# Kernel tuning notes

Hardware: AMD Instinct MI355X
Metric: run time of the kernel (lower is better)

## Reference

```python
import jax, jax.numpy as jnp
import numpy as np

B, C, H, W = 16, 512, 64, 64

def setup_inputs() -> dict:
    key = jax.random.key(0)
    k1, k2, k3 = jax.random.split(key, 3)
    x = jax.random.normal(k1, (B, C, H, W), dtype=jnp.float32)
    gamma = jnp.zeros((1,), dtype=jnp.float32)
    W1 = jax.random.normal(k2, (C, C // 8), dtype=jnp.float32) * (1.0 / np.sqrt(C))
    b1 = jnp.zeros((C // 8,), dtype=jnp.float32)
    W2 = jax.random.normal(k3, (C // 8, C), dtype=jnp.float32) * (1.0 / np.sqrt(C // 8))
    b2 = jnp.zeros((C,), dtype=jnp.float32)
    return {"x": x, "gamma": gamma, "W1": W1, "b1": b1, "W2": W2, "b2": b2}

def reference(x, gamma, W1, b1, W2, b2):
    b, c, h, w = x.shape
    q = x.reshape(b, c, h * w)                      # B,C,HW
    energy = jnp.einsum('bcn,bdn->bcd', q, q)       # B,C,C
    energy_new = jnp.max(energy, axis=-1, keepdims=True) - energy
    attention = jax.nn.softmax(energy_new, axis=-1)
    ch_out = jnp.einsum('bcd,bdn->bcn', attention, q).reshape(b, c, h, w)
    # SE branch: global avg pool -> Linear -> ReLU -> Linear -> Sigmoid
    se = jnp.mean(x, axis=(2, 3))                   # B,C
    se = jax.nn.relu(se @ W1 + b1)
    se = jax.nn.sigmoid(se @ W2 + b2)               # B,C
    out = gamma * (ch_out * se[:, :, None, None]) + x
    return out
```

## Files before the change

kernel.cpp:

```cpp
#include <hip/hip_runtime.h>
#include <cstdint>
#include <cstddef>

#define B_ 16
#define C_ 512
#define N_ 4096
#define CH_ 64

#define VMWAIT(n) asm volatile("s_waitcnt vmcnt(" #n ")" ::: "memory")
#define LGKM0()   asm volatile("s_waitcnt lgkmcnt(0)" ::: "memory")
#define BARRAW()  asm volatile("s_barrier" ::: "memory")
#define SCHEDBAR() __builtin_amdgcn_sched_barrier(0)

typedef __attribute__((ext_vector_type(8))) short short8;
typedef __attribute__((ext_vector_type(4))) short short4t;
typedef __attribute__((ext_vector_type(4))) float f32x4;

__device__ __forceinline__ unsigned short f2bf(float f) {
  union { float f; unsigned u; } v; v.f = f;
  unsigned r = v.u + 0x7FFFu + ((v.u >> 16) & 1u);
  return (unsigned short)(r >> 16);
}
__device__ __forceinline__ float bf2f(unsigned short u) {
  union { unsigned u; float f; } v; v.u = ((unsigned)u) << 16;
  return v.f;
}
__device__ __forceinline__ ushort4 cvt4(float4 v) {
  ushort4 u; u.x = f2bf(v.x); u.y = f2bf(v.y); u.z = f2bf(v.z); u.w = f2bf(v.w);
  return u;
}
__device__ __forceinline__ void gload_lds16(const void* g, void* l) {
  __builtin_amdgcn_global_load_lds((__attribute__((address_space(1))) void*)g,
                                   (__attribute__((address_space(3))) void*)l,
                                   16, 0, 0);
}
__device__ __forceinline__ unsigned lds_off(const void* p) {
  return (unsigned)(size_t)(__attribute__((address_space(3))) const char*)p;
}

template <int CPW>
__device__ __forceinline__ void stage_pair(
    const unsigned short* __restrict__ Asrc, const unsigned short* __restrict__ Bsrc,
    char* Adst, char* Bdst, int t, int ko, bool doB) {
  const int l = t & 63, wid = t >> 6;
  const int srow = l >> 3, scc = l & 7;
#pragma unroll
  for (int i = 0; i < CPW; ++i) {
    const int chunk = wid * CPW + i;
    const int row = chunk * 8 + srow;
    const int cc = scc ^ (row & 7);
    gload_lds16(Asrc + (size_t)row * N_ + ko + cc * 8, Adst + chunk * 1024);
    if (doB)
      gload_lds16(Bsrc + (size_t)row * N_ + ko + cc * 8, Bdst + chunk * 1024);
  }
}
template <int MF, int NF>
__device__ __forceinline__ void gemm_step_t(const char* Abase, const char* Bbase,
                                            int l, int wA, int wB,
                                            f32x4 (&acc)[MF][NF]) {
#pragma unroll
  for (int ks = 0; ks < 2; ++ks) {
    short8 af[MF], bfv[NF];
#pragma unroll
    for (int m = 0; m < MF; ++m) {
      const int row = wA * (MF * 16) + m * 16 + (l & 15);
      const int ch = (ks * 4 + (l >> 4)) ^ (row & 7);
      af[m] = *(const short8*)(Abase + row * 128 + ch * 16);
    }
#pragma unroll
    for (int n = 0; n < NF; ++n) {
      const int row = wB * (NF * 16) + n * 16 + (l & 15);
      const int ch = (ks * 4 + (l >> 4)) ^ (row & 7);
      bfv[n] = *(const short8*)(Bbase + row * 128 + ch * 16);
    }
#pragma unroll
    for (int m = 0; m < MF; ++m)
#pragma unroll
      for (int n = 0; n < NF; ++n)
        acc[m][n] = __builtin_amdgcn_mfma_f32_16x16x32_bf16(af[m], bfv[n],
                                                            acc[m][n], 0, 0, 0);
  }
}

__device__ __forceinline__ void stage_att_half(
    const unsigned short* __restrict__ src, char* dst, int t, int ko, int h) {
  const int l = t & 63, wid = t >> 6;
  const int srow = l >> 3, scc = l & 7;
#pragma unroll
  for (int i = 0; i < 2; ++i) {
    const int chunk = h * 16 + wid * 2 + i;
    const int row = chunk * 8 + srow;
    const int cc = scc ^ (row & 7);
    gload_lds16(src + (size_t)row * C_ + ko + cc * 8, dst + chunk * 1024);
  }
}
__device__ __forceinline__ void stage_q_half(
    const unsigned short* __restrict__ src,
    char* dst, int t, int h) {
  const int l = t & 63, wid = t >> 6;
  const int dd = (l >> 1) & 3;
  const int nb = (l >> 3) * 16 + (l & 1) * 8;
#pragma unroll
  for (int i = 0; i < 2; ++i) {
    const int chunk = h * 16 + wid * 2 + i;
    gload_lds16(src + (size_t)((chunk >> 1) * 4 + dd) * N_ + (chunk & 1) * 128 + nb,
                dst + chunk * 1024);
  }
}

template <int KS>
__device__ __forceinline__ void load_af(const char* Qc, int l, int wn2,
                                        short4t (&lo)[8], short4t (&hi)[8]) {
  const unsigned base = lds_off(Qc) + KS * 16384 + (unsigned)((l >> 4) * 4096 +
                        wn2 * 1024 + (l & 15) * 2);
#pragma unroll
  for (int nf = 0; nf < 8; ++nf) {
    const unsigned a = base + nf * 128;
    asm volatile("ds_read_b64_tr_b16 %0, %2\n\t"
                 "ds_read_b64_tr_b16 %1, %2 offset:2048"
                 : "=&v"(lo[nf]), "=&v"(hi[nf]) : "v"(a));
  }
}
template <int KS, int CB>
__device__ __forceinline__ void load_bf(const char* Pc, int l, int wc,
                                        short8 (&bf)[2]) {
#pragma unroll
  for (int cf = 0; cf < 2; ++cf) {
    const int c_l = CB * 128 + wc * 32 + cf * 16 + (l & 15);
    bf[cf] = *(const short8*)(Pc + c_l * 128 +
                              (((KS * 4 + (l >> 4)) ^ (c_l & 7)) * 16));
  }
}
template <int CB>
__device__ __forceinline__ void mfma16(const short8 (&af)[8], const short8 (&bf)[2],
                                       f32x4 (&acc)[8][4]) {
  __builtin_amdgcn_s_setprio(1);
#pragma unroll
  for (int nf = 0; nf < 8; ++nf)
#pragma unroll
    for (int cf = 0; cf < 2; ++cf)
      acc[nf][CB * 2 + cf] = __builtin_amdgcn_mfma_f32_16x16x32_bf16(
          af[nf], bf[cf], acc[nf][CB * 2 + cf], 0, 0, 0);
  __builtin_amdgcn_s_setprio(0);
}

__global__ __launch_bounds__(256) void k1_convert(
    const float* __restrict__ x, unsigned short* __restrict__ qbf,
    float* __restrict__ partial) {
  __shared__ float wsum[4];
  const size_t base = (size_t)blockIdx.x * N_;
  const int t = threadIdx.x;
  float s = 0.f;
#pragma unroll
  for (int k = 0; k < 4; ++k) {
    const int idx = (t + k * 256) * 4;
    float4 v = *(const float4*)(x + base + idx);
    *(ushort4*)(qbf + base + idx) = cvt4(v);
    s += (v.x + v.y) + (v.z + v.w);
  }
#pragma unroll
  for (int o = 1; o < 64; o <<= 1) s += __shfl_xor(s, o);
  if ((t & 63) == 0) wsum[t >> 6] = s;
  __syncthreads();
  if (t == 0) partial[blockIdx.x] = (wsum[0] + wsum[1]) + (wsum[2] + wsum[3]);
}

__global__ __launch_bounds__(256) void k2_se(
    const float* __restrict__ partial, const float* __restrict__ gamma,
    const float* __restrict__ W1, const float* __restrict__ b1,
    const float* __restrict__ W2, const float* __restrict__ b2,
    float* __restrict__ gse) {
  __shared__ float se_s[C_];
  __shared__ float hp[4][CH_];
  __shared__ float h_s[CH_];
  const int b = blockIdx.x, t = threadIdx.x;
  for (int c = t; c < C_; c += 256)
    se_s[c] = partial[b * C_ + c] * (1.0f / (float)N_);
  __syncthreads();
  {
    const int h = t & 63, seg = t >> 6;
    float a = 0.f;
    const int cb = seg * 128;
    for (int c = cb; c < cb + 128; ++c) a += se_s[c] * W1[c * CH_ + h];
    hp[seg][h] = a;
  }
  __syncthreads();
  if (t < CH_) {
    float a = b1[t] + hp[0][t] + hp[1][t] + hp[2][t] + hp[3][t];
    h_s[t] = fmaxf(a, 0.f);
  }
  __syncthreads();
  const float g = gamma[0];
  for (int c = t; c < C_; c += 256) {
    float a = b2[c];
#pragma unroll
    for (int hh = 0; hh < CH_; ++hh) a += h_s[hh] * W2[hh * C_ + c];
    const float sig = 1.0f / (1.0f + __expf(-a));
    gse[b * C_ + c] = g * sig;
  }
}

__global__ __launch_bounds__(512) void k3_energy(
    const unsigned short* __restrict__ qbf, float* __restrict__ ep) {
  __shared__ alignas(16) char lds[65536];
  const int orig = blockIdx.x;
  const int wg = (orig & 7) * 80 + (orig >> 3);
  const int b = wg / 40;
  const int rem = wg % 40;
  const int kc = rem / 10;
  const int tid = rem % 10;
  int i, j;
  if (tid < 4)      { i = 0; j = tid; }
  else if (tid < 7) { i = 1; j = tid - 3; }
  else if (tid < 9) { i = 2; j = tid - 5; }
  else              { i = 3; j = 3; }
  const int c0 = i * 128, d0 = j * 128;
  const bool diag = (i == j);
  const unsigned short* qb = qbf + (size_t)b * C_ * N_ + kc * 1024;
  const int t = threadIdx.x, l = t & 63, wid = t >> 6;
  const int wd = wid >> 1, wcc = wid & 1;
  f32x4 acc[2][4];
#pragma unroll
  for (int m = 0; m < 2; ++m)
#pragma unroll
    for (int n = 0; n < 4; ++n) acc[m][n] = (f32x4){0.f, 0.f, 0.f, 0.f};
  char* A0 = lds;             char* B0 = lds + 16384;
  char* A1 = lds + 32768;     char* B1 = lds + 49152;
  const unsigned short* cp = qb + (size_t)c0 * N_;
  const unsigned short* dp = qb + (size_t)d0 * N_;

  stage_pair<2>(cp, dp, A0, B0, t, 0, !diag);
  for (int kt = 0; kt < 16; ++kt) {
    char* curA = (kt & 1) ? A1 : A0;
    char* curB = (kt & 1) ? B1 : B0;
    char* nxtA = (kt & 1) ? A0 : A1;
    char* nxtB = (kt & 1) ? B0 : B1;
    if (kt < 15) {
      stage_pair<2>(cp, dp, nxtA, nxtB, t, (kt + 1) * 64, !diag);
      if (diag) { VMWAIT(2); } else { VMWAIT(4); }
    } else {
      VMWAIT(0);
    }
    BARRAW();
    gemm_step_t<2, 4>(diag ? curA : curB, curA, l, wd, wcc, acc);
    BARRAW();
  }

  float* Lf = (float*)lds;
  float* eb = ep + ((size_t)(kc * B_ + b)) * C_ * C_;
#pragma unroll
  for (int df = 0; df < 2; ++df)
#pragma unroll
    for (int cf = 0; cf < 4; ++cf) {
      const int c_l = wcc * 64 + cf * 16 + (l & 15);
      const int d4 = wd * 32 + df * 16 + ((l >> 4) << 2);
      *(float4*)&Lf[c_l * 128 + (d4 ^ ((c_l & 7) << 2))] =
          *(const float4*)&acc[df][cf];
    }
  __syncthreads();
#pragma unroll
  for (int jj = 0; jj < 8; ++jj) {
    const int row = jj * 16 + (t >> 5);
    const int col4 = (t & 31) * 4;
    float4 v = *(const float4*)&Lf[row * 128 + (col4 ^ ((row & 7) << 2))];
    *(float4*)&eb[(size_t)(c0 + row) * C_ + d0 + col4] = v;
  }
  if (!diag) {
    __syncthreads();
#pragma unroll
    for (int df = 0; df < 2; ++df)
#pragma unroll
      for (int cf = 0; cf < 4; ++cf) {
        const int c_l = wcc * 64 + cf * 16 + (l & 15);
#pragma unroll
        for (int r = 0; r < 4; ++r) {
          const int d_l = wd * 32 + df * 16 + ((l >> 4) << 2) + r;
          Lf[d_l * 128 + (c_l ^ ((d_l & 7) << 2))] = acc[df][cf][r];
        }
      }
    __syncthreads();
#pragma unroll
    for (int jj = 0; jj < 8; ++jj) {
      const int row = jj * 16 + (t >> 5);
      const int col4 = (t & 31) * 4;
      float4 v = *(const float4*)&Lf[row * 128 + (col4 ^ ((row & 7) << 2))];
      *(float4*)&eb[(size_t)(d0 + row) * C_ + c0 + col4] = v;
    }
  }
}

__global__ __launch_bounds__(256) void k4_softmax(const float* __restrict__ ep,
                                                  unsigned short* __restrict__ att) {
  const int t = threadIdx.x, l = t & 63, wid = t >> 6;
  const size_t row = (size_t)blockIdx.x * 4 + wid;
  f32x4 v0 = (f32x4){0.f, 0.f, 0.f, 0.f}, v1 = v0;
#pragma unroll
  for (int k = 0; k < 4; ++k) {
    const f32x4* er = (const f32x4*)(ep + ((size_t)k * B_ * C_ + row) * C_);
    v0 += er[l];
    v1 += er[64 + l];
  }
  float mn = fminf(fminf(fminf(v0[0], v0[1]), fminf(v0[2], v0[3])),
                   fminf(fminf(v1[0], v1[1]), fminf(v1[2], v1[3])));
#pragma unroll
  for (int s = 1; s < 64; s <<= 1) mn = fminf(mn, __shfl_xor(mn, s));
  float e0 = __expf(mn - v0[0]), e1 = __expf(mn - v0[1]);
  float e2 = __expf(mn - v0[2]), e3 = __expf(mn - v0[3]);
  float e4 = __expf(mn - v1[0]), e5 = __expf(mn - v1[1]);
  float e6 = __expf(mn - v1[2]), e7 = __expf(mn - v1[3]);
  float sm = ((e0 + e1) + (e2 + e3)) + ((e4 + e5) + (e6 + e7));
#pragma unroll
  for (int s = 1; s < 64; s <<= 1) sm += __shfl_xor(sm, s);
  const float inv = 1.0f / sm;
  unsigned short* ar = att + row * C_;
  ushort4 u0, u1;
  u0.x = f2bf(e0 * inv); u0.y = f2bf(e1 * inv);
  u0.z = f2bf(e2 * inv); u0.w = f2bf(e3 * inv);
  u1.x = f2bf(e4 * inv); u1.y = f2bf(e5 * inv);
  u1.z = f2bf(e6 * inv); u1.w = f2bf(e7 * inv);
  *(ushort4*)(ar + 4 * l) = u0;
  *(ushort4*)(ar + 256 + 4 * l) = u1;
}

__global__ __launch_bounds__(512) void k5_pv(
    const unsigned short* __restrict__ att, const unsigned short* __restrict__ qbf,
    const float* __restrict__ gse, float* __restrict__ out) {
  __shared__ alignas(16) char lds[131072];
  const int orig = blockIdx.x;
  const int wg = (orig & 7) * 64 + (orig >> 3);
  const int b = wg >> 5;
  const int rem = wg & 31;
  const int c0 = (rem & 1) * 256, n0 = (rem >> 1) * 256;
  const int t = threadIdx.x, l = t & 63, wid = t >> 6;
  const int wn2 = wid >> 2, wc = wid & 3;
  const unsigned short* ab = att + (size_t)b * C_ * C_ + (size_t)c0 * C_;
  const unsigned short* qb = qbf + (size_t)b * C_ * N_ + n0;
  f32x4 acc[8][4];
#pragma unroll
  for (int m = 0; m < 8; ++m)
#pragma unroll
    for (int n = 0; n < 4; ++n) acc[m][n] = (f32x4){0.f, 0.f, 0.f, 0.f};
  char* P0 = lds;            char* P1 = lds + 32768;
  char* Q0 = lds + 65536;    char* Q1 = lds + 98304;

  short4t lo[8], hi[8];
  short8 af[8], bf[2];

  stage_att_half(ab, P0, t, 0, 0);
  stage_att_half(ab, P0, t, 0, 1);
  stage_q_half(qb, Q0, t, 0);
  stage_q_half(qb, Q0, t, 1);

  for (int kt = 0; kt < 8; ++kt) {
    const char* Pc = (kt & 1) ? P1 : P0;
    const char* Qc = (kt & 1) ? Q1 : Q0;
    char* Pn = (kt & 1) ? P0 : P1;
    char* Qn = (kt & 1) ? Q0 : Q1;
    const int ko = (kt + 1) * 64;
    const unsigned short* qn = qb + (size_t)ko * N_;
    VMWAIT(2);
    BARRAW();
    load_af<0>(Qc, l, wn2, lo, hi);
    load_bf<0, 0>(Pc, l, wc, bf);
    if (kt < 7) stage_att_half(ab, Pn, t, ko, 0);
    LGKM0(); SCHEDBAR();
#pragma unroll
    for (int nf = 0; nf < 8; ++nf)
      af[nf] = __builtin_shufflevector(lo[nf], hi[nf], 0, 1, 2, 3, 4, 5, 6, 7);
    mfma16<0>(af, bf, acc);
    load_bf<0, 1>(Pc, l, wc, bf);
    if (kt < 7) stage_att_half(ab, Pn, t, ko, 1);
    LGKM0(); SCHEDBAR();
    mfma16<1>(af, bf, acc);
    if (kt < 7) { VMWAIT(4); } else { VMWAIT(0); }
    BARRAW();
    load_af<1>(Qc, l, wn2, lo, hi);
    load_bf<1, 1>(Pc, l, wc, bf);
    if (kt < 7) stage_q_half(qn, Qn, t, 0);
    LGKM0(); SCHEDBAR();
#pragma unroll
    for (int nf = 0; nf < 8; ++nf)
      af[nf] = __builtin_shufflevector(lo[nf], hi[nf], 0, 1, 2, 3, 4, 5, 6, 7);
    mfma16<1>(af, bf, acc);
    load_bf<1, 0>(Pc, l, wc, bf);
    if (kt < 7) stage_q_half(qn, Qn, t, 1);
    LGKM0(); SCHEDBAR();
    mfma16<0>(af, bf, acc);
  }

  float* Lf = (float*)lds;
  const unsigned short* xb = qbf + (size_t)b * C_ * N_;
  float* ob = out + (size_t)b * C_ * N_;
  const float* gseb = gse + b * C_;
  const int g16 = l >> 4;
#pragma unroll
  for (int s = 0; s < 2; ++s) {
    BARRAW();
    if (wn2 == s) {
#pragma unroll
      for (int nf = 0; nf < 8; ++nf)
#pragma unroll
        for (int j = 0; j < 4; ++j) {
          const int c_l = (j >> 1) * 128 + wc * 32 + (j & 1) * 16 + (l & 15);
          const int n4 = nf * 16 + g16 * 4;
          *(float4*)&Lf[c_l * 128 + (n4 ^ ((c_l & 7) << 2))] =
              *(const float4*)&acc[nf][j];
        }
    }
    BARRAW();
#pragma unroll
    for (int it = 0; it < 16; ++it) {
      const int row = it * 16 + (t >> 5);
      const int col4 = (t & 31) * 4;
      const int c = c0 + row;
      const float g = gseb[c];
      float4 v = *(const float4*)&Lf[row * 128 + (col4 ^ ((row & 7) << 2))];
      const size_t gofs = (size_t)c * N_ + n0 + s * 128 + col4;
      ushort4 xu = *(const ushort4*)(xb + gofs);
      float4 ov;
      ov.x = g * v.x + bf2f(xu.x);
      ov.y = g * v.y + bf2f(xu.y);
      ov.z = g * v.z + bf2f(xu.z);
      ov.w = g * v.w + bf2f(xu.w);
      *(float4*)(ob + gofs) = ov;
    }
  }
}

extern "C" void kernel_launch(void* const* d_in, const int* in_sizes, int n_in,
                              void* d_out, int out_size, void* d_ws, size_t ws_size,
                              hipStream_t stream) {
  (void)in_sizes; (void)n_in; (void)out_size; (void)ws_size;
  const float* x     = (const float*)d_in[0];
  const float* gamma = (const float*)d_in[1];
  const float* W1    = (const float*)d_in[2];
  const float* b1    = (const float*)d_in[3];
  const float* W2    = (const float*)d_in[4];
  const float* b2    = (const float*)d_in[5];
  float* out = (float*)d_out;
  char* ws = (char*)d_ws;

  unsigned short* qbf     = (unsigned short*)(ws);
  unsigned short* att     = (unsigned short*)(ws + 67108864);
  float*          partial = (float*)(ws + 75497472);
  float*          gse     = (float*)(ws + 75530240);
  float* epartial = out;

  k1_convert<<<dim3(B_ * C_), dim3(256), 0, stream>>>(x, qbf, partial);
  k2_se<<<dim3(B_), dim3(256), 0, stream>>>(partial, gamma, W1, b1, W2, b2, gse);
  k3_energy<<<dim3(640), dim3(512), 0, stream>>>(qbf, epartial);
  k4_softmax<<<dim3(B_ * C_ / 4), dim3(256), 0, stream>>>(epartial, att);
  k5_pv<<<dim3(512), dim3(512), 0, stream>>>(att, qbf, gse, out);
}
```

Measured before the change: 189.8 us.

## Restructure energy GEMM into full 256x256 tiles reusing the PV pipeline

The energy kernel used to compute only upper-triangular 128x128 tiles with a mirrored transpose store. It now computes all four 256x256 tiles per batch and K-chunk with 256 workgroups, each using the deeper double-buffered 8x4 MFMA pipeline from the PV kernel and a new A-staging layout. This raises MFMA work per LDS load and cuts the number of workgroups. The cost is redundant computation of symmetric blocks (16 tiles instead of 10 per batch and chunk), 128KB of LDS per block and lower occupancy.

```diff
diff --git a/kernel.cpp b/kernel.cpp
--- a/kernel.cpp
+++ b/kernel.cpp
@@ -38,51 +38,8 @@
   return (unsigned)(size_t)(__attribute__((address_space(3))) const char*)p;
 }
 
-template <int CPW>
-__device__ __forceinline__ void stage_pair(
-    const unsigned short* __restrict__ Asrc, const unsigned short* __restrict__ Bsrc,
-    char* Adst, char* Bdst, int t, int ko, bool doB) {
-  const int l = t & 63, wid = t >> 6;
-  const int srow = l >> 3, scc = l & 7;
-#pragma unroll
-  for (int i = 0; i < CPW; ++i) {
-    const int chunk = wid * CPW + i;
-    const int row = chunk * 8 + srow;
-    const int cc = scc ^ (row & 7);
-    gload_lds16(Asrc + (size_t)row * N_ + ko + cc * 8, Adst + chunk * 1024);
-    if (doB)
-      gload_lds16(Bsrc + (size_t)row * N_ + ko + cc * 8, Bdst + chunk * 1024);
-  }
-}
-template <int MF, int NF>
-__device__ __forceinline__ void gemm_step_t(const char* Abase, const char* Bbase,
-                                            int l, int wA, int wB,
-                                            f32x4 (&acc)[MF][NF]) {
-#pragma unroll
-  for (int ks = 0; ks < 2; ++ks) {
-    short8 af[MF], bfv[NF];
-#pragma unroll
-    for (int m = 0; m < MF; ++m) {
-      const int row = wA * (MF * 16) + m * 16 + (l & 15);
-      const int ch = (ks * 4 + (l >> 4)) ^ (row & 7);
-      af[m] = *(const short8*)(Abase + row * 128 + ch * 16);
-    }
-#pragma unroll
-    for (int n = 0; n < NF; ++n) {
-      const int row = wB * (NF * 16) + n * 16 + (l & 15);
-      const int ch = (ks * 4 + (l >> 4)) ^ (row & 7);
-      bfv[n] = *(const short8*)(Bbase + row * 128 + ch * 16);
-    }
-#pragma unroll
-    for (int m = 0; m < MF; ++m)
-#pragma unroll
-      for (int n = 0; n < NF; ++n)
-        acc[m][n] = __builtin_amdgcn_mfma_f32_16x16x32_bf16(af[m], bfv[n],
-                                                            acc[m][n], 0, 0, 0);
-  }
-}
-
-__device__ __forceinline__ void stage_att_half(
+template <int STRIDE>
+__device__ __forceinline__ void stage_rows_half(
     const unsigned short* __restrict__ src, char* dst, int t, int ko, int h) {
   const int l = t & 63, wid = t >> 6;
   const int srow = l >> 3, scc = l & 7;
@@ -91,12 +48,56 @@
     const int chunk = h * 16 + wid * 2 + i;
     const int row = chunk * 8 + srow;
     const int cc = scc ^ (row & 7);
-    gload_lds16(src + (size_t)row * C_ + ko + cc * 8, dst + chunk * 1024);
-  }
-}
+    gload_lds16(src + (size_t)row * STRIDE + ko + cc * 8, dst + chunk * 1024);
+  }
+}
+template <int KS, int CB>
+__device__ __forceinline__ void load_bf(const char* Pc, int l, int wc,
+                                        short8 (&bf)[2]) {
+#pragma unroll
+  for (int cf = 0; cf < 2; ++cf) {
+    const int c_l = CB * 128 + wc * 32 + cf * 16 + (l & 15);
+    bf[cf] = *(const short8*)(Pc + c_l * 128 +
+                              (((KS * 4 + (l >> 4)) ^ (c_l & 7)) * 16));
+  }
+}
+
+__device__ __forceinline__ void stage_a_half(
+    const unsigned short* __restrict__ src,
+    char* dst, int t, int ko, int h) {
+  const int r = t & 255;
+  const int gb = t >> 8;
+#pragma unroll
+  for (int i = 0; i < 2; ++i) {
+    const int g = gb + 2 * i;
+    gload_lds16(src + (size_t)r * N_ + ko + h * 32 + g * 8,
+                dst + h * 16384 + g * 4096 + r * 16);
+  }
+}
+template <int KS>
+__device__ __forceinline__ void load_af3(const char* A, int l, int wd2,
+                                         short8 (&af)[8]) {
+  const char* base = A + KS * 16384 + (l >> 4) * 4096 +
+                     (wd2 * 128 + (l & 15)) * 16;
+#pragma unroll
+  for (int nf = 0; nf < 8; ++nf)
+    af[nf] = *(const short8*)(base + nf * 256);
+}
+template <int CB>
+__device__ __forceinline__ void mfma16(const short8 (&af)[8], const short8 (&bf)[2],
+                                       f32x4 (&acc)[8][4]) {
+  __builtin_amdgcn_s_setprio(1);
+#pragma unroll
+  for (int nf = 0; nf < 8; ++nf)
+#pragma unroll
+    for (int cf = 0; cf < 2; ++cf)
+      acc[nf][CB * 2 + cf] = __builtin_amdgcn_mfma_f32_16x16x32_bf16(
+          af[nf], bf[cf], acc[nf][CB * 2 + cf], 0, 0, 0);
+  __builtin_amdgcn_s_setprio(0);
+}
+
 __device__ __forceinline__ void stage_q_half(
-    const unsigned short* __restrict__ src,
-    char* dst, int t, int h) {
+    const unsigned short* __restrict__ src, char* dst, int t, int h) {
   const int l = t & 63, wid = t >> 6;
   const int dd = (l >> 1) & 3;
   const int nb = (l >> 3) * 16 + (l & 1) * 8;
@@ -107,7 +108,6 @@
                 dst + chunk * 1024);
   }
 }
-
 template <int KS>
 __device__ __forceinline__ void load_af(const char* Qc, int l, int wn2,
                                         short4t (&lo)[8], short4t (&hi)[8]) {
@@ -120,28 +120,6 @@
                  "ds_read_b64_tr_b16 %1, %2 offset:2048"
                  : "=&v"(lo[nf]), "=&v"(hi[nf]) : "v"(a));
   }
-}
-template <int KS, int CB>
-__device__ __forceinline__ void load_bf(const char* Pc, int l, int wc,
-                                        short8 (&bf)[2]) {
-#pragma unroll
-  for (int cf = 0; cf < 2; ++cf) {
-    const int c_l = CB * 128 + wc * 32 + cf * 16 + (l & 15);
-    bf[cf] = *(const short8*)(Pc + c_l * 128 +
-                              (((KS * 4 + (l >> 4)) ^ (c_l & 7)) * 16));
-  }
-}
-template <int CB>
-__device__ __forceinline__ void mfma16(const short8 (&af)[8], const short8 (&bf)[2],
-                                       f32x4 (&acc)[8][4]) {
-  __builtin_amdgcn_s_setprio(1);
-#pragma unroll
-  for (int nf = 0; nf < 8; ++nf)
-#pragma unroll
-    for (int cf = 0; cf < 2; ++cf)
-      acc[nf][CB * 2 + cf] = __builtin_amdgcn_mfma_f32_16x16x32_bf16(
-          af[nf], bf[cf], acc[nf][CB * 2 + cf], 0, 0, 0);
-  __builtin_amdgcn_s_setprio(0);
 }
 
 __global__ __launch_bounds__(256) void k1_convert(
@@ -202,89 +180,87 @@
 
 __global__ __launch_bounds__(512) void k3_energy(
     const unsigned short* __restrict__ qbf, float* __restrict__ ep) {
-  __shared__ alignas(16) char lds[65536];
+  __shared__ alignas(16) char lds[131072];
   const int orig = blockIdx.x;
-  const int wg = (orig & 7) * 80 + (orig >> 3);
-  const int b = wg / 40;
-  const int rem = wg % 40;
-  const int kc = rem / 10;
-  const int tid = rem % 10;
-  int i, j;
-  if (tid < 4)      { i = 0; j = tid; }
-  else if (tid < 7) { i = 1; j = tid - 3; }
-  else if (tid < 9) { i = 2; j = tid - 5; }
-  else              { i = 3; j = 3; }
-  const int c0 = i * 128, d0 = j * 128;
-  const bool diag = (i == j);
+  const int assign = (orig & 7) * 32 + (orig >> 3);
+  const int b = assign >> 4;
+  const int rem = assign & 15;
+  const int kc = rem >> 2;
+  const int d0 = ((rem >> 1) & 1) * 256, c0 = (rem & 1) * 256;
   const unsigned short* qb = qbf + (size_t)b * C_ * N_ + kc * 1024;
+  const unsigned short* ap = qb + (size_t)d0 * N_;
+  const unsigned short* bp = qb + (size_t)c0 * N_;
   const int t = threadIdx.x, l = t & 63, wid = t >> 6;
-  const int wd = wid >> 1, wcc = wid & 1;
-  f32x4 acc[2][4];
-#pragma unroll
-  for (int m = 0; m < 2; ++m)
+  const int wd2 = wid >> 2, wc = wid & 3;
+  f32x4 acc[8][4];
+#pragma unroll
+  for (int m = 0; m < 8; ++m)
 #pragma unroll
     for (int n = 0; n < 4; ++n) acc[m][n] = (f32x4){0.f, 0.f, 0.f, 0.f};
-  char* A0 = lds;             char* B0 = lds + 16384;
-  char* A1 = lds + 32768;     char* B1 = lds + 49152;
-  const unsigned short* cp = qb + (size_t)c0 * N_;
-  const unsigned short* dp = qb + (size_t)d0 * N_;
-
-  stage_pair<2>(cp, dp, A0, B0, t, 0, !diag);
+  char* P0 = lds;            char* P1 = lds + 32768;
+  char* Q0 = lds + 65536;    char* Q1 = lds + 98304;
+
+  short8 af[8], bf[2];
+
+  stage_rows_half<N_>(bp, P0, t, 0, 0);
+  stage_rows_half<N_>(bp, P0, t, 0, 1);
+  stage_a_half(ap, Q0, t, 0, 0);
+  stage_a_half(ap, Q0, t, 0, 1);
+
   for (int kt = 0; kt < 16; ++kt) {
-    char* curA = (kt & 1) ? A1 : A0;
-    char* curB = (kt & 1) ? B1 : B0;
-    char* nxtA = (kt & 1) ? A0 : A1;
-    char* nxtB = (kt & 1) ? B0 : B1;
-    if (kt < 15) {
-      stage_pair<2>(cp, dp, nxtA, nxtB, t, (kt + 1) * 64, !diag);
-      if (diag) { VMWAIT(2); } else { VMWAIT(4); }
-    } else {
-      VMWAIT(0);
-    }
-    BARRAW();
-    gemm_step_t<2, 4>(diag ? curA : curB, curA, l, wd, wcc, acc);
-    BARRAW();
+    const char* Pc = (kt & 1) ? P1 : P0;
+    const char* Qc = (kt & 1) ? Q1 : Q0;
+    char* Pn = (kt & 1) ? P0 : P1;
+    char* Qn = (kt & 1) ? Q0 : Q1;
+    const int ko = (kt + 1) * 64;
+    VMWAIT(2);
+    BARRAW();
+    load_af3<0>(Qc, l, wd2, af);
+    load_bf<0, 0>(Pc, l, wc, bf);
+    if (kt < 15) stage_rows_half<N_>(bp, Pn, t, ko, 0);
+    LGKM0(); SCHEDBAR();
+    mfma16<0>(af, bf, acc);
+    load_bf<0, 1>(Pc, l, wc, bf);
+    if (kt < 15) stage_rows_half<N_>(bp, Pn, t, ko, 1);
+    LGKM0(); SCHEDBAR();
+    mfma16<1>(af, bf, acc);
+    if (kt < 15) { VMWAIT(4); } else { VMWAIT(0); }
+    BARRAW();
+    load_af3<1>(Qc, l, wd2, af);
+    load_bf<1, 1>(Pc, l, wc, bf);
+    if (kt < 15) stage_a_half(ap, Qn, t, ko, 0);
+    LGKM0(); SCHEDBAR();
+    mfma16<1>(af, bf, acc);
+    load_bf<1, 0>(Pc, l, wc, bf);
+    if (kt < 15) stage_a_half(ap, Qn, t, ko, 1);
+    LGKM0(); SCHEDBAR();
+    mfma16<0>(af, bf, acc);
   }
 
   float* Lf = (float*)lds;
   float* eb = ep + ((size_t)(kc * B_ + b)) * C_ * C_;
-#pragma unroll
-  for (int df = 0; df < 2; ++df)
-#pragma unroll
-    for (int cf = 0; cf < 4; ++cf) {
-      const int c_l = wcc * 64 + cf * 16 + (l & 15);
-      const int d4 = wd * 32 + df * 16 + ((l >> 4) << 2);
-      *(float4*)&Lf[c_l * 128 + (d4 ^ ((c_l & 7) << 2))] =
-          *(const float4*)&acc[df][cf];
+  const int g16 = l >> 4;
+#pragma unroll
+  for (int s = 0; s < 2; ++s) {
+    BARRAW();
+    if (wd2 == s) {
+#pragma unroll
+      for (int nf = 0; nf < 8; ++nf)
+#pragma unroll
+        for (int j = 0; j < 4; ++j) {
+          const int c_l = (j >> 1) * 128 + wc * 32 + (j & 1) * 16 + (l & 15);
+          const int d4 = nf * 16 + g16 * 4;
+          *(float4*)&Lf[c_l * 128 + (d4 ^ ((c_l & 7) << 2))] =
+              *(const float4*)&acc[nf][j];
+        }
     }
-  __syncthreads();
-#pragma unroll
-  for (int jj = 0; jj < 8; ++jj) {
-    const int row = jj * 16 + (t >> 5);
-    const int col4 = (t & 31) * 4;
-    float4 v = *(const float4*)&Lf[row * 128 + (col4 ^ ((row & 7) << 2))];
-    *(float4*)&eb[(size_t)(c0 + row) * C_ + d0 + col4] = v;
-  }
-  if (!diag) {
-    __syncthreads();
-#pragma unroll
-    for (int df = 0; df < 2; ++df)
-#pragma unroll
-      for (int cf = 0; cf < 4; ++cf) {
-        const int c_l = wcc * 64 + cf * 16 + (l & 15);
-#pragma unroll
-        for (int r = 0; r < 4; ++r) {
-          const int d_l = wd * 32 + df * 16 + ((l >> 4) << 2) + r;
-          Lf[d_l * 128 + (c_l ^ ((d_l & 7) << 2))] = acc[df][cf][r];
-        }
-      }
-    __syncthreads();
-#pragma unroll
-    for (int jj = 0; jj < 8; ++jj) {
-      const int row = jj * 16 + (t >> 5);
+    BARRAW();
+#pragma unroll
+    for (int it = 0; it < 16; ++it) {
+      const int row = it * 16 + (t >> 5);
       const int col4 = (t & 31) * 4;
       float4 v = *(const float4*)&Lf[row * 128 + (col4 ^ ((row & 7) << 2))];
-      *(float4*)&eb[(size_t)(d0 + row) * C_ + c0 + col4] = v;
+      *(float4*)&eb[(size_t)(c0 + row) * C_ + d0 + s * 128 + col4] = v;
     }
   }
 }
@@ -346,8 +322,8 @@
   short4t lo[8], hi[8];
   short8 af[8], bf[2];
 
-  stage_att_half(ab, P0, t, 0, 0);
-  stage_att_half(ab, P0, t, 0, 1);
+  stage_rows_half<C_>(ab, P0, t, 0, 0);
+  stage_rows_half<C_>(ab, P0, t, 0, 1);
   stage_q_half(qb, Q0, t, 0);
   stage_q_half(qb, Q0, t, 1);
 
@@ -362,14 +338,14 @@
     BARRAW();
     load_af<0>(Qc, l, wn2, lo, hi);
     load_bf<0, 0>(Pc, l, wc, bf);
-    if (kt < 7) stage_att_half(ab, Pn, t, ko, 0);
+    if (kt < 7) stage_rows_half<C_>(ab, Pn, t, ko, 0);
     LGKM0(); SCHEDBAR();
 #pragma unroll
     for (int nf = 0; nf < 8; ++nf)
       af[nf] = __builtin_shufflevector(lo[nf], hi[nf], 0, 1, 2, 3, 4, 5, 6, 7);
     mfma16<0>(af, bf, acc);
     load_bf<0, 1>(Pc, l, wc, bf);
-    if (kt < 7) stage_att_half(ab, Pn, t, ko, 1);
+    if (kt < 7) stage_rows_half<C_>(ab, Pn, t, ko, 1);
     LGKM0(); SCHEDBAR();
     mfma16<1>(af, bf, acc);
     if (kt < 7) { VMWAIT(4); } else { VMWAIT(0); }
@@ -448,7 +424,7 @@
 
   k1_convert<<<dim3(B_ * C_), dim3(256), 0, stream>>>(x, qbf, partial);
   k2_se<<<dim3(B_), dim3(256), 0, stream>>>(partial, gamma, W1, b1, W2, b2, gse);
-  k3_energy<<<dim3(640), dim3(512), 0, stream>>>(qbf, epartial);
+  k3_energy<<<dim3(256), dim3(512), 0, stream>>>(qbf, epartial);
   k4_softmax<<<dim3(B_ * C_ / 4), dim3(256), 0, stream>>>(epartial, att);
   k5_pv<<<dim3(512), dim3(512), 0, stream>>>(att, qbf, gse, out);
 }
```

After: 192.5 us. Within noise of the previous version (+1.4%).
